# Kernel optimization log

Measured on AMD Instinct MI355X. Metric: run time of the kernel, lower is better.

The kernel has to match this reference:

```python
import jax, jax.numpy as jnp
import numpy as np

B, C, H, W = 16, 192, 96, 96
L = 60  # number of stanh quantization levels (codebook size)


def setup_inputs() -> dict:
    key = jax.random.key(0)
    k1, k2, k3 = jax.random.split(key, 3)
    # latent y (pre-quantization) -- scaled so it spans the codebook range
    inputs = jax.random.normal(k1, (B, C, H, W), dtype=jnp.float32) * 5.0
    means = jax.random.normal(k2, (B, C, H, W), dtype=jnp.float32)
    # sorted unique quantization levels (stanh.unique_values); strictly increasing
    base = jnp.linspace(-15.0, 15.0, L, dtype=jnp.float32)
    jitter = jax.random.normal(k3, (L,), dtype=jnp.float32) * 0.05
    codebook = jnp.sort(base + jitter).astype(jnp.float32)
    return {"inputs": inputs, "means": means, "codebook": codebook}


def reference(inputs, means, codebook):
    """quantize(mode='symbols') + dequantize of GaussianConditionalStanh.

    Original: per-element Python loop calling transform_map, i.e.
    argmin_l |codebook[l] - (x - mean)| -> int symbol; dequantize gathers
    codebook[symbol] and adds the mean back (removing_mean=True).
    Vectorized here as a searchsorted over codebook midpoints (exact
    nearest neighbor for a sorted 1-D codebook).
    """
    y = inputs - means                              # [B,C,H,W]
    mid = 0.5 * (codebook[:-1] + codebook[1:])      # [L-1] decision boundaries
    idx = jnp.searchsorted(mid, y)                  # nearest-level index in [0, L)
    symbols = idx.astype(jnp.int32)                 # integer symbols
    dequant = jnp.take(codebook, idx) + means       # map_cdf_sos gather + means
    return symbols, dequant
```

## Files before the change

### kernel.cpp

```cpp
#include <hip/hip_runtime.h>


namespace {

constexpr int kL = 60;
constexpr int kMid = kL - 1;

__global__ __launch_bounds__(256) void stanh_quant_kernel(
    const float* __restrict__ x,
    const float* __restrict__ mean,
    const float* __restrict__ cb,
    float* __restrict__ sym_out,
    float* __restrict__ deq_out,
    int n4)
{
    __shared__ float cb_lds[kL];
    if (threadIdx.x < kL) cb_lds[threadIdx.x] = cb[threadIdx.x];
    __syncthreads();

    float mid[kMid];
#pragma unroll
    for (int i = 0; i < kMid; ++i) mid[i] = 0.5f * (cb[i] + cb[i + 1]);

    const float4* __restrict__ x4 = (const float4*)x;
    const float4* __restrict__ m4 = (const float4*)mean;
    float4* __restrict__ s4 = (float4*)sym_out;
    float4* __restrict__ d4 = (float4*)deq_out;

    const int stride = gridDim.x * blockDim.x;
    for (int g = blockIdx.x * blockDim.x + threadIdx.x; g < n4; g += stride) {
        const float4 xv = x4[g];
        const float4 mv = m4[g];
        const float y0 = xv.x - mv.x;
        const float y1 = xv.y - mv.y;
        const float y2 = xv.z - mv.z;
        const float y3 = xv.w - mv.w;

        int i0 = 0, i1 = 0, i2 = 0, i3 = 0;
#pragma unroll
        for (int i = 0; i < kMid; ++i) {
            i0 += (y0 > mid[i]);
            i1 += (y1 > mid[i]);
            i2 += (y2 > mid[i]);
            i3 += (y3 > mid[i]);
        }

        float4 sv;
        sv.x = (float)i0; sv.y = (float)i1; sv.z = (float)i2; sv.w = (float)i3;
        float4 dv;
        dv.x = cb_lds[i0] + mv.x;
        dv.y = cb_lds[i1] + mv.y;
        dv.z = cb_lds[i2] + mv.z;
        dv.w = cb_lds[i3] + mv.w;

        s4[g] = sv;
        d4[g] = dv;
    }
}

}

extern "C" void kernel_launch(void* const* d_in, const int* in_sizes, int n_in,
                              void* d_out, int out_size, void* d_ws, size_t ws_size,
                              hipStream_t stream) {
    const float* x    = (const float*)d_in[0];
    const float* mean = (const float*)d_in[1];
    const float* cb   = (const float*)d_in[2];

    const int n = in_sizes[0];
    float* sym_out = (float*)d_out;
    float* deq_out = sym_out + n;

    const int n4 = n / 4;
    const int block = 256;
    int grid = 8192;
    const int max_grid = (n4 + block - 1) / block;
    if (grid > max_grid) grid = max_grid;

    hipLaunchKernelGGL(stanh_quant_kernel, dim3(grid), dim3(block), 0, stream,
                       x, mean, cb, sym_out, deq_out, n4);
}
```

Baseline: 386.8 us.

## Replace linear midpoint scan with interpolated guess plus local correction

Swaps the 59-comparison linear count per element for an initial index estimated by linear interpolation across the codebook range, followed by short while-loop corrections against padded midpoints in LDS. Sentinel infinities bound the search. The aim is to cut the ALU cost that made the kernel compute-bound. In exchange it adds data-dependent divergent loops and LDS reads, and the index is only exact if the corrections converge, which they should for a near-uniform codebook.

```diff
diff --git a/kernel.cpp b/kernel.cpp
--- a/kernel.cpp
+++ b/kernel.cpp
@@ -1,10 +1,20 @@
 #include <hip/hip_runtime.h>
+#include <math.h>
 
 
 namespace {
 
 constexpr int kL = 60;
-constexpr int kMid = kL - 1;
+
+__device__ __forceinline__ int find_idx(float y, const float* __restrict__ ms,
+                                        float c0, float invd) {
+    float t = (y - c0) * invd + 0.5f;
+    int g = (int)t;
+    g = max(0, min(g, kL - 1));
+    while (y > ms[g + 1]) ++g;
+    while (y <= ms[g]) --g;
+    return g;
+}
 
 __global__ __launch_bounds__(256) void stanh_quant_kernel(
     const float* __restrict__ x,
@@ -14,13 +24,18 @@
     float* __restrict__ deq_out,
     int n4)
 {
-    __shared__ float cb_lds[kL];
-    if (threadIdx.x < kL) cb_lds[threadIdx.x] = cb[threadIdx.x];
+    __shared__ float cb_s[kL];
+    __shared__ float ms[kL + 4];
+
+    const int tid = threadIdx.x;
+    if (tid < kL) cb_s[tid] = cb[tid];
+    if (tid == 0) ms[0] = -INFINITY;
+    if (tid < kL - 1) ms[tid + 1] = 0.5f * (cb[tid] + cb[tid + 1]);
+    if (tid >= kL - 1 && tid < kL + 3) ms[tid + 1] = INFINITY;
     __syncthreads();
 
-    float mid[kMid];
-#pragma unroll
-    for (int i = 0; i < kMid; ++i) mid[i] = 0.5f * (cb[i] + cb[i + 1]);
+    const float c0 = cb[0];
+    const float invd = 59.0f / (cb[kL - 1] - c0);
 
     const float4* __restrict__ x4 = (const float4*)x;
     const float4* __restrict__ m4 = (const float4*)mean;
@@ -28,7 +43,7 @@
     float4* __restrict__ d4 = (float4*)deq_out;
 
     const int stride = gridDim.x * blockDim.x;
-    for (int g = blockIdx.x * blockDim.x + threadIdx.x; g < n4; g += stride) {
+    for (int g = blockIdx.x * blockDim.x + tid; g < n4; g += stride) {
         const float4 xv = x4[g];
         const float4 mv = m4[g];
         const float y0 = xv.x - mv.x;
@@ -36,22 +51,18 @@
         const float y2 = xv.z - mv.z;
         const float y3 = xv.w - mv.w;
 
-        int i0 = 0, i1 = 0, i2 = 0, i3 = 0;
-#pragma unroll
-        for (int i = 0; i < kMid; ++i) {
-            i0 += (y0 > mid[i]);
-            i1 += (y1 > mid[i]);
-            i2 += (y2 > mid[i]);
-            i3 += (y3 > mid[i]);
-        }
+        const int i0 = find_idx(y0, ms, c0, invd);
+        const int i1 = find_idx(y1, ms, c0, invd);
+        const int i2 = find_idx(y2, ms, c0, invd);
+        const int i3 = find_idx(y3, ms, c0, invd);
 
         float4 sv;
         sv.x = (float)i0; sv.y = (float)i1; sv.z = (float)i2; sv.w = (float)i3;
         float4 dv;
-        dv.x = cb_lds[i0] + mv.x;
-        dv.y = cb_lds[i1] + mv.y;
-        dv.z = cb_lds[i2] + mv.z;
-        dv.w = cb_lds[i3] + mv.w;
+        dv.x = cb_s[i0] + mv.x;
+        dv.y = cb_s[i1] + mv.y;
+        dv.z = cb_s[i2] + mv.z;
+        dv.w = cb_s[i3] + mv.w;
 
         s4[g] = sv;
         d4[g] = dv;
```

Result: faster. 372.4 us (-3.7%).
